# Kernel optimization log

Measured on AMD Instinct MI355X. Metric: run time of the kernel, lower is better.

The kernel has to match this reference:

```python
import jax, jax.numpy as jnp
import numpy as np

N_QUBITS = 8
N_WORDS = 16
DEGREE = 3
N_ANSATZ_LAYERS = 2
VOCAB = 50257
EMB = 512
BATCH = 16
N_ROTS = 4 * N_QUBITS * N_ANSATZ_LAYERS  # 64
DIM = 2 ** N_QUBITS


def _ry_mat(th):
    # [[cos, -sin],[sin, cos]] on theta/2, batched over leading dim
    c = jnp.cos(th / 2).astype(jnp.complex64)
    s = jnp.sin(th / 2).astype(jnp.complex64)
    return jnp.stack([jnp.stack([c, -s], -1), jnp.stack([s, c], -1)], -2)


def _rx_mat(th):
    # [[cos, -i sin],[-i sin, cos]] on theta/2
    c = jnp.cos(th / 2).astype(jnp.complex64)
    s = jnp.sin(th / 2).astype(jnp.complex64)
    return jnp.stack([jnp.stack([c, -1j * s], -1), jnp.stack([-1j * s, c], -1)], -2)


def _apply_1q(st, M, w):
    # st: [BB, 2^n] complex, M: [BB,2,2]; wire 0 is the most-significant axis (tq convention)
    BB = st.shape[0]
    s = st.reshape(BB, 2 ** w, 2, -1)
    s = jnp.einsum('bij,bljr->blir', M, s)
    return s.reshape(BB, -1)


def _apply_ctrl(st, M, c, t, n):
    # controlled-1q gate: apply M on target t only in the control=1 subspace
    BB = st.shape[0]
    full = st.reshape((BB,) + (2,) * n)
    s0 = jnp.take(full, 0, axis=c + 1)
    s1 = jnp.take(full, 1, axis=c + 1)
    ta = (t if t < c else t - 1) + 1  # target axis after removing control axis
    s1 = jnp.moveaxis(s1, ta, -1)
    s1 = jnp.einsum('bij,b...j->b...i', M, s1)
    s1 = jnp.moveaxis(s1, -1, ta)
    return jnp.stack([s0, s1], axis=c + 1).reshape(BB, -1)


def _sim14(st, params, n, layers):
    # circuit-14 ansatz: ry ring, crx down-ring, ry ring, crx up-ring (per layer)
    idx = 0
    for _ in range(layers):
        for i in range(n):
            st = _apply_1q(st, _ry_mat(params[:, idx]), i); idx += 1
        for i in range(n - 1, -1, -1):
            st = _apply_ctrl(st, _rx_mat(params[:, idx]), i, (i + 1) % n, n); idx += 1
        for i in range(n):
            st = _apply_1q(st, _ry_mat(params[:, idx]), i); idx += 1
        for i in [n - 1] + list(range(n - 1)):
            st = _apply_ctrl(st, _rx_mat(params[:, idx]), i, (i - 1) % n, n); idx += 1
    return st


def _apply_unitaries(base, wparams, coeffs):
    # base: [B, DIM]; wparams: [B, W, N_ROTS]; coeffs: [B, W] complex -> LCU sum_w c_w U_w |psi>
    B, W = wparams.shape[0], wparams.shape[1]
    rep = jnp.repeat(base, W, axis=0)  # matches torch repeat(1,W).view(-1,DIM)
    st = _sim14(rep, wparams.reshape(B * W, -1), N_QUBITS, N_ANSATZ_LAYERS)
    return jnp.einsum('bwi,bw->bi', st.reshape(B, W, DIM), coeffs)


def _measure_xyz(st, n):
    # Pauli X/Y/Z expectations per wire; order: [x_0..x_{n-1}, y_..., z_...]
    BB = st.shape[0]
    xs, ys, zs = [], [], []
    for w in range(n):
        s = st.reshape(BB, 2 ** w, 2, -1)
        a0, a1 = s[:, :, 0, :], s[:, :, 1, :]
        cross = jnp.sum(jnp.conj(a0) * a1, axis=(1, 2))
        xs.append(2 * jnp.real(cross))
        ys.append(2 * jnp.imag(cross))
        zs.append(jnp.sum(jnp.abs(a0) ** 2 - jnp.abs(a1) ** 2, axis=(1, 2)))
    return jnp.concatenate([jnp.stack(xs, -1), jnp.stack(ys, -1), jnp.stack(zs, -1)], axis=-1)


def reference(x, embedding_W, emb2rot_W, emb2rot_b, poly_coeffs, mix_coeffs_ri, qff_params, ff1_W, ff1_b, ff2_W, ff2_b):
    B = x.shape[0]
    mix = (mix_coeffs_ri[:, 0] + 1j * mix_coeffs_ri[:, 1]).astype(jnp.complex64)
    coeffs = mix / jnp.maximum(jnp.sum(jnp.abs(mix)), 1e-12)  # L1 normalize
    coeffs = jnp.broadcast_to(coeffs[None, :], (B, N_WORDS))
    emb = embedding_W[x]                       # [B, W, EMB]
    wparams = emb @ emb2rot_W.T + emb2rot_b    # [B, W, N_ROTS]; dropout is identity in eval
    base = jnp.zeros((B, DIM), jnp.complex64).at[:, 0].set(1.0)
    acc = poly_coeffs[0] * base
    work = base
    for d in range(1, DEGREE + 1):
        work = _apply_unitaries(work, wparams, coeffs)
        acc = acc + poly_coeffs[d] * work
    mixed = acc / jnp.sum(jnp.abs(poly_coeffs))
    final_probs = jnp.linalg.norm(mixed, axis=-1)
    normed = mixed / jnp.maximum(final_probs, 1e-12)[:, None]
    qp = jnp.broadcast_to(qff_params[None, :4 * N_QUBITS], (B, 4 * N_QUBITS))  # qff uses 1 layer
    st = _sim14(normed, qp, N_QUBITS, 1)
    exps = _measure_xyz(st, N_QUBITS)          # [B, 3*n_qubits]
    h = jax.nn.relu(exps @ ff1_W.T + ff1_b)
    op = h @ ff2_W.T + ff2_b
    return op, jnp.mean(final_probs)


def setup_inputs():
    key = jax.random.key(0)
    ks = jax.random.split(key, 12)
    x = jax.random.randint(ks[0], (BATCH, N_WORDS), 0, VOCAB)
    embedding_W = jax.random.normal(ks[1], (VOCAB, EMB), jnp.float32) * 0.02
    emb2rot_W = jax.random.normal(ks[2], (N_ROTS, EMB), jnp.float32) * (1.0 / np.sqrt(EMB))
    emb2rot_b = jax.random.normal(ks[3], (N_ROTS,), jnp.float32) * 0.01
    poly_coeffs = jax.random.uniform(ks[4], (DEGREE + 1,), jnp.float32)
    mix_coeffs_ri = jax.random.uniform(ks[5], (N_WORDS, 2), jnp.float32)
    qff_params = jax.random.uniform(ks[6], (N_ROTS,), jnp.float32)
    NM = 3 * N_QUBITS
    ff1_W = jax.random.normal(ks[7], (EMB, NM), jnp.float32) * (1.0 / np.sqrt(NM))
    ff1_b = jnp.zeros((EMB,), jnp.float32)
    ff2_W = jax.random.normal(ks[8], (VOCAB, EMB), jnp.float32) * (1.0 / np.sqrt(EMB))
    ff2_b = jnp.zeros((VOCAB,), jnp.float32)
    return {"x": x, "embedding_W": embedding_W, "emb2rot_W": emb2rot_W, "emb2rot_b": emb2rot_b,
            "poly_coeffs": poly_coeffs, "mix_coeffs_ri": mix_coeffs_ri, "qff_params": qff_params,
            "ff1_W": ff1_W, "ff1_b": ff1_b, "ff2_W": ff2_W, "ff2_b": ff2_b}
```

## Files before the change

### kernel.cpp

```cpp
#include <hip/hip_runtime.h>
#include <hip/hip_bf16.h>

#define NQ 8
#define DIM 256
#define NB 16
#define NW 16
#define VOCABN 50257
#define EMBN 512

__device__ __forceinline__ float2 shfl2(float2 a, int m){
  float2 r; r.x = __shfl_xor(a.x, m, 64); r.y = __shfl_xor(a.y, m, 64); return r;
}
__device__ __forceinline__ float wave_sum(float x){
  #pragma unroll
  for (int off = 1; off < 64; off <<= 1) x += __shfl_xor(x, off, 64);
  return x;
}

__device__ __forceinline__ void ry_pair(float2& a0, float2& a1, float c, float s){
  float2 n0 = make_float2(c*a0.x - s*a1.x, c*a0.y - s*a1.y);
  float2 n1 = make_float2(s*a0.x + c*a1.x, s*a0.y + c*a1.y);
  a0 = n0; a1 = n1;
}
__device__ __forceinline__ void rx_pair(float2& a0, float2& a1, float c, float s){
  float2 n0 = make_float2(c*a0.x + s*a1.y, c*a0.y - s*a1.x);
  float2 n1 = make_float2(c*a1.x + s*a0.y, c*a1.y - s*a0.x);
  a0 = n0; a1 = n1;
}

__device__ __forceinline__ void apply_gate(float2 v[4], int lane, int kind, int cbit, int tbit,
                                           float c, float s){
  if (kind == 0){
    if (tbit == 7){ ry_pair(v[0], v[2], c, s); ry_pair(v[1], v[3], c, s); }
    else if (tbit == 6){ ry_pair(v[0], v[1], c, s); ry_pair(v[2], v[3], c, s); }
    else {
      int m = 1 << tbit;
      #pragma unroll
      for (int r = 0; r < 4; ++r){
        float2 w = shfl2(v[r], m);
        float sg = (lane & m) ? s : -s;
        v[r] = make_float2(c*v[r].x + sg*w.x, c*v[r].y + sg*w.y);
      }
    }
  } else {
    if (tbit >= 6){
      if (cbit >= 6){
        if (cbit == 7) rx_pair(v[2], v[3], c, s);
        else           rx_pair(v[1], v[3], c, s);
      } else {
        int cm = 1 << cbit;
        if (lane & cm){
          if (tbit == 7){ rx_pair(v[0], v[2], c, s); rx_pair(v[1], v[3], c, s); }
          else          { rx_pair(v[0], v[1], c, s); rx_pair(v[2], v[3], c, s); }
        }
      }
    } else {
      int m = 1 << tbit;
      if (cbit >= 6){
        int r0 = (cbit == 6) ? 1 : 2;
        float2 w0 = shfl2(v[r0], m);
        float2 w1 = shfl2(v[3], m);
        v[r0] = make_float2(c*v[r0].x + s*w0.y, c*v[r0].y - s*w0.x);
        v[3]  = make_float2(c*v[3].x  + s*w1.y, c*v[3].y  - s*w1.x);
      } else {
        int cm = 1 << cbit;
        bool act = (lane & cm) != 0;
        #pragma unroll
        for (int r = 0; r < 4; ++r){
          float2 w = shfl2(v[r], m);
          if (act) v[r] = make_float2(c*v[r].x + s*w.y, c*v[r].y - s*w.x);
        }
      }
    }
  }
}

__device__ __forceinline__ void sim32(float2 v[4], int lane, const float2* __restrict__ cs){
  constexpr int KIND[32] = {0,0,0,0,0,0,0,0, 1,1,1,1,1,1,1,1, 0,0,0,0,0,0,0,0, 1,1,1,1,1,1,1,1};
  constexpr int CB[32]   = {0,0,0,0,0,0,0,0, 0,1,2,3,4,5,6,7, 0,0,0,0,0,0,0,0, 0,7,6,5,4,3,2,1};
  constexpr int TB[32]   = {7,6,5,4,3,2,1,0, 7,0,1,2,3,4,5,6, 7,6,5,4,3,2,1,0, 1,0,7,6,5,4,3,2};
  #pragma unroll
  for (int g = 0; g < 32; ++g){
    float2 p = cs[g];
    apply_gate(v, lane, KIND[g], CB[g], TB[g], p.x, p.y);
  }
}

__device__ __forceinline__ void measure_one(const float2 v[4], int lane, int t,
                                            float& xr, float& xi, float& zz){
  xr = 0.f; xi = 0.f; zz = 0.f;
  if (t == 7){
    #pragma unroll
    for (int r = 0; r < 2; ++r){
      float2 a0 = v[r], a1 = v[r+2];
      xr += a0.x*a1.x + a0.y*a1.y;
      xi += a0.x*a1.y - a0.y*a1.x;
      zz += (a0.x*a0.x + a0.y*a0.y) - (a1.x*a1.x + a1.y*a1.y);
    }
  } else if (t == 6){
    #pragma unroll
    for (int r = 0; r < 4; r += 2){
      float2 a0 = v[r], a1 = v[r+1];
      xr += a0.x*a1.x + a0.y*a1.y;
      xi += a0.x*a1.y - a0.y*a1.x;
      zz += (a0.x*a0.x + a0.y*a0.y) - (a1.x*a1.x + a1.y*a1.y);
    }
  } else {
    int m = 1 << t;
    #pragma unroll
    for (int r = 0; r < 4; ++r){
      float2 a = v[r];
      float2 w = shfl2(a, m);
      if (!(lane & m)){
        xr += a.x*w.x + a.y*w.y;
        xi += a.x*w.y - a.y*w.x;
        zz += (a.x*a.x + a.y*a.y) - (w.x*w.x + w.y*w.y);
      }
    }
  }
  xr = wave_sum(xr); xi = wave_sum(xi); zz = wave_sum(zz);
}

__global__ __launch_bounds__(64) void k_prep(
    const int* __restrict__ x, const float* __restrict__ embW,
    const float* __restrict__ e2rW, const float* __restrict__ e2rb,
    const float* __restrict__ mixri, const float* __restrict__ qff,
    float* __restrict__ wcs, float* __restrict__ coeffs, float* __restrict__ qcs)
{
  const int p = blockIdx.x;
  const int j = threadIdx.x;
  const int tok = x[p];
  const float4* er = (const float4*)(embW + (size_t)tok * EMBN);
  const float4* wr = (const float4*)(e2rW + (size_t)j * EMBN);
  float acc = e2rb[j];
  #pragma unroll 4
  for (int k = 0; k < EMBN/4; ++k){
    float4 e = er[k], w4 = wr[k];
    acc += e.x*w4.x + e.y*w4.y + e.z*w4.z + e.w*w4.w;
  }
  float th = 0.5f * acc;
  wcs[(p*64 + j)*2 + 0] = cosf(th);
  wcs[(p*64 + j)*2 + 1] = sinf(th);
  if (p == 0){
    if (j < 32){ float t = 0.5f * qff[j]; qcs[2*j] = cosf(t); qcs[2*j+1] = sinf(t); }
    if (j < 16){
      float ssum = 0.f;
      for (int i = 0; i < 16; ++i){
        float mr = mixri[2*i], mi = mixri[2*i+1];
        ssum += sqrtf(mr*mr + mi*mi);
      }
      ssum = fmaxf(ssum, 1e-12f);
      coeffs[2*j]   = mixri[2*j]   / ssum;
      coeffs[2*j+1] = mixri[2*j+1] / ssum;
    }
  }
}

__global__ __launch_bounds__(64) void k_deg1(
    const float* __restrict__ wcs, const float* __restrict__ coeffs,
    float2* __restrict__ S1)
{
  const int p = blockIdx.x, lane = threadIdx.x;
  const float2* mycs = ((const float2*)wcs) + p*64;
  float2 v[4];
  v[0] = make_float2(lane == 0 ? 1.f : 0.f, 0.f);
  v[1] = v[2] = v[3] = make_float2(0.f, 0.f);
  sim32(v, lane, mycs);
  sim32(v, lane, mycs + 32);
  const float2 coef = ((const float2*)coeffs)[p & 15];
  #pragma unroll
  for (int r = 0; r < 4; ++r){
    float2 a = v[r];
    S1[p*DIM + ((r<<6) | lane)] = make_float2(coef.x*a.x - coef.y*a.y, coef.x*a.y + coef.y*a.x);
  }
}

__global__ __launch_bounds__(64) void k_deg(
    const float2* __restrict__ Sin, float2* __restrict__ Sout,
    const float* __restrict__ wcs, const float* __restrict__ coeffs,
    const float* __restrict__ poly, float2* __restrict__ accs, int dprev)
{
  const int p = blockIdx.x, lane = threadIdx.x;
  const int b = p >> 4, w = p & 15;
  float2 v[4];
  v[0] = v[1] = v[2] = v[3] = make_float2(0.f, 0.f);
  const float2* base = Sin + b*NW*DIM;
  #pragma unroll
  for (int ww = 0; ww < NW; ++ww){
    #pragma unroll
    for (int r = 0; r < 4; ++r){
      float2 a = base[ww*DIM + ((r<<6) | lane)];
      v[r].x += a.x; v[r].y += a.y;
    }
  }
  if (w == 0){
    const float pd = poly[dprev];
    #pragma unroll
    for (int r = 0; r < 4; ++r){
      const int idx = (r<<6) | lane;
      float2 cur = make_float2(pd*v[r].x, pd*v[r].y);
      if (dprev == 1){
        if (idx == 0) cur.x += poly[0];
        accs[b*DIM + idx] = cur;
      } else {
        float2 old = accs[b*DIM + idx];
        accs[b*DIM + idx] = make_float2(old.x + cur.x, old.y + cur.y);
      }
    }
  }
  const float2* mycs = ((const float2*)wcs) + p*64;
  sim32(v, lane, mycs);
  sim32(v, lane, mycs + 32);
  const float2 coef = ((const float2*)coeffs)[w];
  #pragma unroll
  for (int r = 0; r < 4; ++r){
    float2 a = v[r];
    Sout[p*DIM + ((r<<6) | lane)] = make_float2(coef.x*a.x - coef.y*a.y, coef.x*a.y + coef.y*a.x);
  }
}

__global__ __launch_bounds__(512) void k_final(
    const float2* __restrict__ Sin, const float2* __restrict__ accs,
    const float* __restrict__ poly, const float* __restrict__ qcs,
    const float* __restrict__ ff1W, const float* __restrict__ ff1b,
    float* __restrict__ hT, float* __restrict__ fprobs)
{
  const int b = blockIdx.x, tid = threadIdx.x;
  const int w = tid >> 6, lane = tid & 63;
  __shared__ float2 work[DIM];
  __shared__ float  red[8];
  __shared__ float  exps[24];
  __shared__ float  inv_s;
  __shared__ float  ff1_lds[EMBN*24];

  {
    const float4* f4 = (const float4*)ff1W;
    float4* d4 = (float4*)ff1_lds;
    #pragma unroll
    for (int i = 0; i < 6; ++i) d4[i*512 + tid] = f4[i*512 + tid];
  }
  const float psum = fabsf(poly[0]) + fabsf(poly[1]) + fabsf(poly[2]) + fabsf(poly[3]);
  float ssl = 0.f;
  if (tid < DIM){
    float2 s = make_float2(0.f, 0.f);
    const float2* base = Sin + b*NW*DIM;
    #pragma unroll
    for (int ww = 0; ww < NW; ++ww){ float2 a = base[ww*DIM + tid]; s.x += a.x; s.y += a.y; }
    float2 ac = accs[b*DIM + tid];
    const float p3 = poly[3];
    s = make_float2((ac.x + p3*s.x)/psum, (ac.y + p3*s.y)/psum);
    work[tid] = s;
    ssl = s.x*s.x + s.y*s.y;
  }
  ssl = wave_sum(ssl);
  if (lane == 0) red[w] = ssl;
  __syncthreads();
  if (tid == 0){
    float fp = sqrtf(red[0] + red[1] + red[2] + red[3]);
    fprobs[b] = fp;
    inv_s = 1.f / fmaxf(fp, 1e-12f);
  }
  __syncthreads();
  {
    const float inv = inv_s;
    float2 v[4];
    #pragma unroll
    for (int r = 0; r < 4; ++r){
      float2 m = work[(r<<6) | lane];
      v[r] = make_float2(m.x*inv, m.y*inv);
    }
    sim32(v, lane, (const float2*)qcs);
    float xr, xi, zz;
    measure_one(v, lane, 7 - w, xr, xi, zz);
    if (lane == 0){ exps[w] = 2.f*xr; exps[8+w] = 2.f*xi; exps[16+w] = zz; }
  }
  __syncthreads();
  float a = ff1b[tid];
  const float* wr = ff1_lds + tid*24;
  #pragma unroll
  for (int m2 = 0; m2 < 24; ++m2) a += exps[m2]*wr[m2];
  hT[tid*NB + b] = fmaxf(a, 0.f);
}

__global__ __launch_bounds__(256) void k_out(
    const float* __restrict__ hT, const float* __restrict__ ff2W,
    const float* __restrict__ ff2b, const float* __restrict__ fprobs,
    float* __restrict__ out)
{
  __shared__ float4 smem[2048];
  const int tid = threadIdx.x;

  if (blockIdx.x == 0 && tid == 0){
    float s = 0.f;
    #pragma unroll
    for (int i = 0; i < 16; ++i) s += fprobs[i];
    out[(size_t)NB*VOCABN] = s * (1.f/16.f);
  }

  {
    const float4* hT4 = (const float4*)hT;
    #pragma unroll
    for (int i = 0; i < 8; ++i) smem[i*256 + tid] = hT4[i*256 + tid];
  }
  __syncthreads();

  const int r = tid & 63;
  const int q = tid >> 6;
  const int row = blockIdx.x*64 + r;
  const bool valid = (row < VOCABN);

  float4 a0 = make_float4(0,0,0,0), a1 = a0, a2 = a0, a3 = a0;

  if (valid){
    const float4* wv = (const float4*)(ff2W + (size_t)row * EMBN) + q*32;
    const int kbase = q*128;
    #pragma unroll 8
    for (int c = 0; c < 32; ++c){
      float4 wq = wv[c];
      const int k0 = (kbase + c*4) << 2;
      float4 h00 = smem[k0+0],  h01 = smem[k0+1],  h02 = smem[k0+2],  h03 = smem[k0+3];
      float4 h10 = smem[k0+4],  h11 = smem[k0+5],  h12 = smem[k0+6],  h13 = smem[k0+7];
      float4 h20 = smem[k0+8],  h21 = smem[k0+9],  h22 = smem[k0+10], h23 = smem[k0+11];
      float4 h30 = smem[k0+12], h31 = smem[k0+13], h32 = smem[k0+14], h33 = smem[k0+15];
      a0.x += wq.x*h00.x + wq.y*h10.x + wq.z*h20.x + wq.w*h30.x;
      a0.y += wq.x*h00.y + wq.y*h10.y + wq.z*h20.y + wq.w*h30.y;
      a0.z += wq.x*h00.z + wq.y*h10.z + wq.z*h20.z + wq.w*h30.z;
      a0.w += wq.x*h00.w + wq.y*h10.w + wq.z*h20.w + wq.w*h30.w;
      a1.x += wq.x*h01.x + wq.y*h11.x + wq.z*h21.x + wq.w*h31.x;
      a1.y += wq.x*h01.y + wq.y*h11.y + wq.z*h21.y + wq.w*h31.y;
      a1.z += wq.x*h01.z + wq.y*h11.z + wq.z*h21.z + wq.w*h31.z;
      a1.w += wq.x*h01.w + wq.y*h11.w + wq.z*h21.w + wq.w*h31.w;
      a2.x += wq.x*h02.x + wq.y*h12.x + wq.z*h22.x + wq.w*h32.x;
      a2.y += wq.x*h02.y + wq.y*h12.y + wq.z*h22.y + wq.w*h32.y;
      a2.z += wq.x*h02.z + wq.y*h12.z + wq.z*h22.z + wq.w*h32.z;
      a2.w += wq.x*h02.w + wq.y*h12.w + wq.z*h22.w + wq.w*h32.w;
      a3.x += wq.x*h03.x + wq.y*h13.x + wq.z*h23.x + wq.w*h33.x;
      a3.y += wq.x*h03.y + wq.y*h13.y + wq.z*h23.y + wq.w*h33.y;
      a3.z += wq.x*h03.z + wq.y*h13.z + wq.z*h23.z + wq.w*h33.z;
      a3.w += wq.x*h03.w + wq.y*h13.w + wq.z*h23.w + wq.w*h33.w;
    }
  }
  __syncthreads();

  if (q > 0){
    smem[0*256 + q*64 + r] = a0;
    smem[1*256 + q*64 + r] = a1;
    smem[2*256 + q*64 + r] = a2;
    smem[3*256 + q*64 + r] = a3;
  }
  __syncthreads();
  if (q == 0 && valid){
    #pragma unroll
    for (int qq = 1; qq < 4; ++qq){
      float4 b0 = smem[0*256 + qq*64 + r], b1 = smem[1*256 + qq*64 + r];
      float4 b2 = smem[2*256 + qq*64 + r], b3 = smem[3*256 + qq*64 + r];
      a0.x += b0.x; a0.y += b0.y; a0.z += b0.z; a0.w += b0.w;
      a1.x += b1.x; a1.y += b1.y; a1.z += b1.z; a1.w += b1.w;
      a2.x += b2.x; a2.y += b2.y; a2.z += b2.z; a2.w += b2.w;
      a3.x += b3.x; a3.y += b3.y; a3.z += b3.z; a3.w += b3.w;
    }
    const float bias = ff2b[row];
    out[(size_t) 0*VOCABN + row] = a0.x + bias;
    out[(size_t) 1*VOCABN + row] = a0.y + bias;
    out[(size_t) 2*VOCABN + row] = a0.z + bias;
    out[(size_t) 3*VOCABN + row] = a0.w + bias;
    out[(size_t) 4*VOCABN + row] = a1.x + bias;
    out[(size_t) 5*VOCABN + row] = a1.y + bias;
    out[(size_t) 6*VOCABN + row] = a1.z + bias;
    out[(size_t) 7*VOCABN + row] = a1.w + bias;
    out[(size_t) 8*VOCABN + row] = a2.x + bias;
    out[(size_t) 9*VOCABN + row] = a2.y + bias;
    out[(size_t)10*VOCABN + row] = a2.z + bias;
    out[(size_t)11*VOCABN + row] = a2.w + bias;
    out[(size_t)12*VOCABN + row] = a3.x + bias;
    out[(size_t)13*VOCABN + row] = a3.y + bias;
    out[(size_t)14*VOCABN + row] = a3.z + bias;
    out[(size_t)15*VOCABN + row] = a3.w + bias;
  }
}

extern "C" void kernel_launch(void* const* d_in, const int* in_sizes, int n_in,
                              void* d_out, int out_size, void* d_ws, size_t ws_size,
                              hipStream_t stream)
{
  const int*   x     = (const int*)  d_in[0];
  const float* embW  = (const float*)d_in[1];
  const float* e2rW  = (const float*)d_in[2];
  const float* e2rb  = (const float*)d_in[3];
  const float* poly  = (const float*)d_in[4];
  const float* mixri = (const float*)d_in[5];
  const float* qff   = (const float*)d_in[6];
  const float* ff1W  = (const float*)d_in[7];
  const float* ff1b  = (const float*)d_in[8];
  const float* ff2W  = (const float*)d_in[9];
  const float* ff2b  = (const float*)d_in[10];
  float* out = (float*)d_out;
  float* ws  = (float*)d_ws;

  float*  wcs    = ws;
  float*  coeffs = ws + 32768;
  float*  qcs    = ws + 32800;
  float*  hT     = ws + 32864;
  float*  fprobs = ws + 41056;
  float2* accs   = (float2*)(ws + 41072);
  float2* S1     = (float2*)(ws + 49264);
  float2* S2     = (float2*)(ws + 180336);

  k_prep <<<256, 64, 0, stream>>>(x, embW, e2rW, e2rb, mixri, qff, wcs, coeffs, qcs);
  k_deg1 <<<256, 64, 0, stream>>>(wcs, coeffs, S1);
  k_deg  <<<256, 64, 0, stream>>>(S1, S2, wcs, coeffs, poly, accs, 1);
  k_deg  <<<256, 64, 0, stream>>>(S2, S1, wcs, coeffs, poly, accs, 2);
  k_final<<<NB, 512, 0, stream>>>(S1, accs, poly, qcs, ff1W, ff1b, hT, fprobs);
  k_out  <<<(VOCABN + 63)/64, 256, 0, stream>>>(hT, ff2W, ff2b, fprobs, out);
}
```

Before: 289.2 us.

## Fuse prep with degree-1 simulation and tile output GEMV two rows per thread

Merges the embedding-to-rotation prep kernel with the first-degree circuit simulation, passing angles through shared memory, and recomputes the mix coefficients inside each kernel. This removes one launch and the global round-trip for the coefficients. The output projection now computes two vocab rows per thread, which halves the block count and reuses each shared-memory load of the hidden state across both rows. The reduction buffer is padded to avoid bank conflicts. In exchange, the output kernel uses more registers, which may lower occupancy on a kernel dominated by memory bandwidth.

```diff
diff --git a/kernel.cpp b/kernel.cpp
--- a/kernel.cpp
+++ b/kernel.cpp
@@ -121,53 +121,50 @@
   xr = wave_sum(xr); xi = wave_sum(xi); zz = wave_sum(zz);
 }
 
-__global__ __launch_bounds__(64) void k_prep(
+__global__ __launch_bounds__(64) void k_pd1(
     const int* __restrict__ x, const float* __restrict__ embW,
     const float* __restrict__ e2rW, const float* __restrict__ e2rb,
     const float* __restrict__ mixri, const float* __restrict__ qff,
-    float* __restrict__ wcs, float* __restrict__ coeffs, float* __restrict__ qcs)
+    float* __restrict__ wcs, float* __restrict__ qcs, float2* __restrict__ S1)
 {
   const int p = blockIdx.x;
   const int j = threadIdx.x;
-  const int tok = x[p];
-  const float4* er = (const float4*)(embW + (size_t)tok * EMBN);
-  const float4* wr = (const float4*)(e2rW + (size_t)j * EMBN);
-  float acc = e2rb[j];
-  #pragma unroll 4
-  for (int k = 0; k < EMBN/4; ++k){
-    float4 e = er[k], w4 = wr[k];
-    acc += e.x*w4.x + e.y*w4.y + e.z*w4.z + e.w*w4.w;
-  }
-  float th = 0.5f * acc;
-  wcs[(p*64 + j)*2 + 0] = cosf(th);
-  wcs[(p*64 + j)*2 + 1] = sinf(th);
-  if (p == 0){
-    if (j < 32){ float t = 0.5f * qff[j]; qcs[2*j] = cosf(t); qcs[2*j+1] = sinf(t); }
-    if (j < 16){
-      float ssum = 0.f;
-      for (int i = 0; i < 16; ++i){
-        float mr = mixri[2*i], mi = mixri[2*i+1];
-        ssum += sqrtf(mr*mr + mi*mi);
-      }
-      ssum = fmaxf(ssum, 1e-12f);
-      coeffs[2*j]   = mixri[2*j]   / ssum;
-      coeffs[2*j+1] = mixri[2*j+1] / ssum;
-    }
-  }
-}
-
-__global__ __launch_bounds__(64) void k_deg1(
-    const float* __restrict__ wcs, const float* __restrict__ coeffs,
-    float2* __restrict__ S1)
-{
-  const int p = blockIdx.x, lane = threadIdx.x;
-  const float2* mycs = ((const float2*)wcs) + p*64;
+  __shared__ float2 cs[64];
+
+  {
+    const int tok = x[p];
+    const float4* er = (const float4*)(embW + (size_t)tok * EMBN);
+    const float4* wr = (const float4*)(e2rW + (size_t)j * EMBN);
+    float acc = e2rb[j];
+    #pragma unroll 4
+    for (int k = 0; k < EMBN/4; ++k){
+      float4 e = er[k], w4 = wr[k];
+      acc += e.x*w4.x + e.y*w4.y + e.z*w4.z + e.w*w4.w;
+    }
+    float th = 0.5f * acc;
+    float2 c2 = make_float2(cosf(th), sinf(th));
+    cs[j] = c2;
+    ((float2*)wcs)[p*64 + j] = c2;
+    if (p == 0 && j < 32){ float t = 0.5f * qff[j]; ((float2*)qcs)[j] = make_float2(cosf(t), sinf(t)); }
+  }
+  __syncthreads();
+
+  const int lane = j;
   float2 v[4];
   v[0] = make_float2(lane == 0 ? 1.f : 0.f, 0.f);
   v[1] = v[2] = v[3] = make_float2(0.f, 0.f);
-  sim32(v, lane, mycs);
-  sim32(v, lane, mycs + 32);
-  const float2 coef = ((const float2*)coeffs)[p & 15];
+  sim32(v, lane, cs);
+  sim32(v, lane, cs + 32);
+
+  float ssum = 0.f;
+  #pragma unroll
+  for (int i = 0; i < 16; ++i){
+    float mr = mixri[2*i], mi = mixri[2*i+1];
+    ssum += sqrtf(mr*mr + mi*mi);
+  }
+  ssum = fmaxf(ssum, 1e-12f);
+  const int w = p & 15;
+  const float2 coef = make_float2(mixri[2*w]/ssum, mixri[2*w+1]/ssum);
   #pragma unroll
   for (int r = 0; r < 4; ++r){
     float2 a = v[r];
@@ -177,7 +174,7 @@
 
 __global__ __launch_bounds__(64) void k_deg(
     const float2* __restrict__ Sin, float2* __restrict__ Sout,
-    const float* __restrict__ wcs, const float* __restrict__ coeffs,
+    const float* __restrict__ wcs, const float* __restrict__ mixri,
     const float* __restrict__ poly, float2* __restrict__ accs, int dprev)
 {
   const int p = blockIdx.x, lane = threadIdx.x;
@@ -211,7 +208,14 @@
   const float2* mycs = ((const float2*)wcs) + p*64;
   sim32(v, lane, mycs);
   sim32(v, lane, mycs + 32);
-  const float2 coef = ((const float2*)coeffs)[w];
+  float ssum = 0.f;
+  #pragma unroll
+  for (int i = 0; i < 16; ++i){
+    float mr = mixri[2*i], mi = mixri[2*i+1];
+    ssum += sqrtf(mr*mr + mi*mi);
+  }
+  ssum = fmaxf(ssum, 1e-12f);
+  const float2 coef = make_float2(mixri[2*w]/ssum, mixri[2*w+1]/ssum);
   #pragma unroll
   for (int r = 0; r < 4; ++r){
     float2 a = v[r];
@@ -287,8 +291,10 @@
     const float* __restrict__ ff2b, const float* __restrict__ fprobs,
     float* __restrict__ out)
 {
-  __shared__ float4 smem[2048];
+  __shared__ float4 hs[2048];
   const int tid = threadIdx.x;
+  const int q = tid >> 6;
+  const int lane = tid & 63;
 
   if (blockIdx.x == 0 && tid == 0){
     float s = 0.f;
@@ -300,82 +306,88 @@
   {
     const float4* hT4 = (const float4*)hT;
     #pragma unroll
-    for (int i = 0; i < 8; ++i) smem[i*256 + tid] = hT4[i*256 + tid];
-  }
-  __syncthreads();
-
-  const int r = tid & 63;
-  const int q = tid >> 6;
-  const int row = blockIdx.x*64 + r;
-  const bool valid = (row < VOCABN);
-
-  float4 a0 = make_float4(0,0,0,0), a1 = a0, a2 = a0, a3 = a0;
-
-  if (valid){
-    const float4* wv = (const float4*)(ff2W + (size_t)row * EMBN) + q*32;
-    const int kbase = q*128;
-    #pragma unroll 8
-    for (int c = 0; c < 32; ++c){
-      float4 wq = wv[c];
-      const int k0 = (kbase + c*4) << 2;
-      float4 h00 = smem[k0+0],  h01 = smem[k0+1],  h02 = smem[k0+2],  h03 = smem[k0+3];
-      float4 h10 = smem[k0+4],  h11 = smem[k0+5],  h12 = smem[k0+6],  h13 = smem[k0+7];
-      float4 h20 = smem[k0+8],  h21 = smem[k0+9],  h22 = smem[k0+10], h23 = smem[k0+11];
-      float4 h30 = smem[k0+12], h31 = smem[k0+13], h32 = smem[k0+14], h33 = smem[k0+15];
-      a0.x += wq.x*h00.x + wq.y*h10.x + wq.z*h20.x + wq.w*h30.x;
-      a0.y += wq.x*h00.y + wq.y*h10.y + wq.z*h20.y + wq.w*h30.y;
-      a0.z += wq.x*h00.z + wq.y*h10.z + wq.z*h20.z + wq.w*h30.z;
-      a0.w += wq.x*h00.w + wq.y*h10.w + wq.z*h20.w + wq.w*h30.w;
-      a1.x += wq.x*h01.x + wq.y*h11.x + wq.z*h21.x + wq.w*h31.x;
-      a1.y += wq.x*h01.y + wq.y*h11.y + wq.z*h21.y + wq.w*h31.y;
-      a1.z += wq.x*h01.z + wq.y*h11.z + wq.z*h21.z + wq.w*h31.z;
-      a1.w += wq.x*h01.w + wq.y*h11.w + wq.z*h21.w + wq.w*h31.w;
-      a2.x += wq.x*h02.x + wq.y*h12.x + wq.z*h22.x + wq.w*h32.x;
-      a2.y += wq.x*h02.y + wq.y*h12.y + wq.z*h22.y + wq.w*h32.y;
-      a2.z += wq.x*h02.z + wq.y*h12.z + wq.z*h22.z + wq.w*h32.z;
-      a2.w += wq.x*h02.w + wq.y*h12.w + wq.z*h22.w + wq.w*h32.w;
-      a3.x += wq.x*h03.x + wq.y*h13.x + wq.z*h23.x + wq.w*h33.x;
-      a3.y += wq.x*h03.y + wq.y*h13.y + wq.z*h23.y + wq.w*h33.y;
-      a3.z += wq.x*h03.z + wq.y*h13.z + wq.z*h23.z + wq.w*h33.z;
-      a3.w += wq.x*h03.w + wq.y*h13.w + wq.z*h23.w + wq.w*h33.w;
-    }
-  }
-  __syncthreads();
-
+    for (int i = 0; i < 8; ++i) hs[i*256 + tid] = hT4[i*256 + tid];
+  }
+  __syncthreads();
+
+  const int base = blockIdx.x * 128;
+  const int r0 = base + lane;
+  const int r1 = r0 + 64;
+  const int rc0 = min(r0, VOCABN-1);
+  const int rc1 = min(r1, VOCABN-1);
+
+  float4 acc0[4], acc1[4];
+  #pragma unroll
+  for (int i = 0; i < 4; ++i){ acc0[i] = make_float4(0,0,0,0); acc1[i] = make_float4(0,0,0,0); }
+
+  const float4* w0 = (const float4*)(ff2W + (size_t)rc0 * EMBN) + q*32;
+  const float4* w1 = (const float4*)(ff2W + (size_t)rc1 * EMBN) + q*32;
+
+  #pragma unroll 4
+  for (int c = 0; c < 32; ++c){
+    float4 wa = w0[c];
+    float4 wb = w1[c];
+    const int k0 = (q*128 + c*4) << 2;
+    #pragma unroll
+    for (int kk = 0; kk < 4; ++kk){
+      const float wka = (kk==0) ? wa.x : (kk==1) ? wa.y : (kk==2) ? wa.z : wa.w;
+      const float wkb = (kk==0) ? wb.x : (kk==1) ? wb.y : (kk==2) ? wb.z : wb.w;
+      #pragma unroll
+      for (int bq = 0; bq < 4; ++bq){
+        float4 hh = hs[k0 + kk*4 + bq];
+        acc0[bq].x += wka*hh.x; acc0[bq].y += wka*hh.y;
+        acc0[bq].z += wka*hh.z; acc0[bq].w += wka*hh.w;
+        acc1[bq].x += wkb*hh.x; acc1[bq].y += wkb*hh.y;
+        acc1[bq].z += wkb*hh.z; acc1[bq].w += wkb*hh.w;
+      }
+    }
+  }
+  __syncthreads();
+
+  float* redf = (float*)hs;
   if (q > 0){
-    smem[0*256 + q*64 + r] = a0;
-    smem[1*256 + q*64 + r] = a1;
-    smem[2*256 + q*64 + r] = a2;
-    smem[3*256 + q*64 + r] = a3;
-  }
-  __syncthreads();
-  if (q == 0 && valid){
-    #pragma unroll
-    for (int qq = 1; qq < 4; ++qq){
-      float4 b0 = smem[0*256 + qq*64 + r], b1 = smem[1*256 + qq*64 + r];
-      float4 b2 = smem[2*256 + qq*64 + r], b3 = smem[3*256 + qq*64 + r];
-      a0.x += b0.x; a0.y += b0.y; a0.z += b0.z; a0.w += b0.w;
-      a1.x += b1.x; a1.y += b1.y; a1.z += b1.z; a1.w += b1.w;
-      a2.x += b2.x; a2.y += b2.y; a2.z += b2.z; a2.w += b2.w;
-      a3.x += b3.x; a3.y += b3.y; a3.z += b3.z; a3.w += b3.w;
-    }
-    const float bias = ff2b[row];
-    out[(size_t) 0*VOCABN + row] = a0.x + bias;
-    out[(size_t) 1*VOCABN + row] = a0.y + bias;
-    out[(size_t) 2*VOCABN + row] = a0.z + bias;
-    out[(size_t) 3*VOCABN + row] = a0.w + bias;
-    out[(size_t) 4*VOCABN + row] = a1.x + bias;
-    out[(size_t) 5*VOCABN + row] = a1.y + bias;
-    out[(size_t) 6*VOCABN + row] = a1.z + bias;
-    out[(size_t) 7*VOCABN + row] = a1.w + bias;
-    out[(size_t) 8*VOCABN + row] = a2.x + bias;
-    out[(size_t) 9*VOCABN + row] = a2.y + bias;
-    out[(size_t)10*VOCABN + row] = a2.z + bias;
-    out[(size_t)11*VOCABN + row] = a2.w + bias;
-    out[(size_t)12*VOCABN + row] = a3.x + bias;
-    out[(size_t)13*VOCABN + row] = a3.y + bias;
-    out[(size_t)14*VOCABN + row] = a3.z + bias;
-    out[(size_t)15*VOCABN + row] = a3.w + bias;
+    float* dst = redf + (q-1)*2112 + lane*33;
+    #pragma unroll
+    for (int bq = 0; bq < 4; ++bq){
+      dst[bq*4+0] = acc0[bq].x; dst[bq*4+1] = acc0[bq].y;
+      dst[bq*4+2] = acc0[bq].z; dst[bq*4+3] = acc0[bq].w;
+      dst[16+bq*4+0] = acc1[bq].x; dst[16+bq*4+1] = acc1[bq].y;
+      dst[16+bq*4+2] = acc1[bq].z; dst[16+bq*4+3] = acc1[bq].w;
+    }
+  }
+  __syncthreads();
+  if (q == 0){
+    #pragma unroll
+    for (int qq = 0; qq < 3; ++qq){
+      const float* src = redf + qq*2112 + lane*33;
+      #pragma unroll
+      for (int bq = 0; bq < 4; ++bq){
+        acc0[bq].x += src[bq*4+0]; acc0[bq].y += src[bq*4+1];
+        acc0[bq].z += src[bq*4+2]; acc0[bq].w += src[bq*4+3];
+        acc1[bq].x += src[16+bq*4+0]; acc1[bq].y += src[16+bq*4+1];
+        acc1[bq].z += src[16+bq*4+2]; acc1[bq].w += src[16+bq*4+3];
+      }
+    }
+    if (r0 < VOCABN){
+      const float bias = ff2b[r0];
+      #pragma unroll
+      for (int bq = 0; bq < 4; ++bq){
+        out[(size_t)(bq*4+0)*VOCABN + r0] = acc0[bq].x + bias;
+        out[(size_t)(bq*4+1)*VOCABN + r0] = acc0[bq].y + bias;
+        out[(size_t)(bq*4+2)*VOCABN + r0] = acc0[bq].z + bias;
+        out[(size_t)(bq*4+3)*VOCABN + r0] = acc0[bq].w + bias;
+      }
+    }
+    if (r1 < VOCABN){
+      const float bias = ff2b[r1];
+      #pragma unroll
+      for (int bq = 0; bq < 4; ++bq){
+        out[(size_t)(bq*4+0)*VOCABN + r1] = acc1[bq].x + bias;
+        out[(size_t)(bq*4+1)*VOCABN + r1] = acc1[bq].y + bias;
+        out[(size_t)(bq*4+2)*VOCABN + r1] = acc1[bq].z + bias;
+        out[(size_t)(bq*4+3)*VOCABN + r1] = acc1[bq].w + bias;
+      }
+    }
   }
 }
 
@@ -398,18 +410,16 @@
   float* ws  = (float*)d_ws;
 
   float*  wcs    = ws;
-  float*  coeffs = ws + 32768;
-  float*  qcs    = ws + 32800;
-  float*  hT     = ws + 32864;
-  float*  fprobs = ws + 41056;
-  float2* accs   = (float2*)(ws + 41072);
-  float2* S1     = (float2*)(ws + 49264);
-  float2* S2     = (float2*)(ws + 180336);
-
-  k_prep <<<256, 64, 0, stream>>>(x, embW, e2rW, e2rb, mixri, qff, wcs, coeffs, qcs);
-  k_deg1 <<<256, 64, 0, stream>>>(wcs, coeffs, S1);
-  k_deg  <<<256, 64, 0, stream>>>(S1, S2, wcs, coeffs, poly, accs, 1);
-  k_deg  <<<256, 64, 0, stream>>>(S2, S1, wcs, coeffs, poly, accs, 2);
+  float*  qcs    = ws + 32768;
+  float*  hT     = ws + 32832;
+  float*  fprobs = ws + 41024;
+  float2* accs   = (float2*)(ws + 41040);
+  float2* S1     = (float2*)(ws + 49232);
+  float2* S2     = (float2*)(ws + 180304);
+
+  k_pd1  <<<256, 64, 0, stream>>>(x, embW, e2rW, e2rb, mixri, qff, wcs, qcs, S1);
+  k_deg  <<<256, 64, 0, stream>>>(S1, S2, wcs, mixri, poly, accs, 1);
+  k_deg  <<<256, 64, 0, stream>>>(S2, S1, wcs, mixri, poly, accs, 2);
   k_final<<<NB, 512, 0, stream>>>(S1, accs, poly, qcs, ff1W, ff1b, hT, fprobs);
-  k_out  <<<(VOCABN + 63)/64, 256, 0, stream>>>(hT, ff2W, ff2b, fprobs, out);
-}
+  k_out  <<<(VOCABN + 127)/128, 256, 0, stream>>>(hT, ff2W, ff2b, fprobs, out);
+}
```

New measurement: 290.0 us. Within noise of the previous version (+0.3%).
